# Kernel tuning notes

Measured on AMD Instinct MI355X. Metric: run time of the kernel, lower is better.

## Reference

```python
import jax, jax.numpy as jnp
import numpy as np

B, S, D = 2, 8192, 1024
H, DK, DV = 8, 64, 64
DH = 4096
SEG = 2048
NSEG = S // SEG
EPS = 1e-5


def setup_inputs() -> dict:
    key = jax.random.key(0)
    ks = jax.random.split(key, 9)
    g = lambda k, shp, sc: jax.random.normal(k, shp, jnp.float32) * sc
    return {
        "x": g(ks[0], (B, S, D), 1.0),
        "Wq": g(ks[1], (D, H * DK), 0.02),
        "Wk": g(ks[2], (D, H * DK), 0.02),
        "Wv": g(ks[3], (D, H * DV), 0.02),
        "Wo": g(ks[4], (H * DV, D), 0.02),
        "betas": g(ks[5], (1, H, 1, DV), 1.0),
        "W1": g(ks[6], (D, DH), 0.02),
        "b1": jnp.zeros((DH,), jnp.float32),
        "W2": g(ks[7], (DH, D), 0.02),
        "b2": jnp.zeros((D,), jnp.float32),
        "ln_g": jnp.ones((D,), jnp.float32),
        "ln_b": jnp.zeros((D,), jnp.float32),
    }


def _compressive_memory(x, Wq, Wk, Wv, Wo, betas):
    # project and split heads: (B, H, S, d)
    q = (x @ Wq).reshape(B, S, H, DK).transpose(0, 2, 1, 3)
    k = (x @ Wk).reshape(B, S, H, DK).transpose(0, 2, 1, 3)
    v = (x @ Wv).reshape(B, S, H, DV).transpose(0, 2, 1, 3)

    # chunk into segments: (NSEG, B, H, SEG, d)
    seg = lambda t, d: t.reshape(B, H, NSEG, SEG, d).transpose(2, 0, 1, 3, 4)
    qs, ks_, vs = seg(q, DK), seg(k, DK), seg(v, DV)

    mem0 = jnp.zeros((B, H, DK, DV), jnp.float32)
    z0 = jnp.ones((B, H, DK, 1), jnp.float32) / DK
    causal_mask = jnp.tril(jnp.ones((SEG, SEG), bool))
    scale = np.float32(1.0 / np.sqrt(DK))
    gate = jax.nn.sigmoid(betas)  # (1, H, 1, DV)

    def step(carry, inp):
        mem, z = carry
        qi, ki, vi = inp  # (B, H, SEG, d)
        sq = jax.nn.elu(qi) + 1.0
        sk = jax.nn.elu(ki) + 1.0
        # memory retrieval (uses state from previous segments)
        att_mem = (sq @ mem) / (sq @ z)  # (B, H, SEG, DV)
        # local causal SDP attention within the segment
        scores = jnp.einsum('bhqd,bhkd->bhqk', qi, ki) * scale
        scores = jnp.where(causal_mask, scores, -jnp.inf)
        att_dot = jax.nn.softmax(scores, axis=-1) @ vi
        # linear memory update
        mem = mem + jnp.einsum('bhsd,bhsv->bhdv', sk, vi)
        z = z + sk.sum(axis=-2, keepdims=True).transpose(0, 1, 3, 2)
        att = gate * att_mem + (1.0 - gate) * att_dot
        return (mem, z), att

    _, atts = jax.lax.scan(step, (mem0, z0), (qs, ks_, vs))
    # (NSEG, B, H, SEG, DV) -> (B, S, H*DV)
    att = atts.transpose(1, 0, 3, 2, 4).reshape(B, S, H * DV)
    return att @ Wo


def reference(x, Wq, Wk, Wv, Wo, betas, W1, b1, W2, b2, ln_g, ln_b):
    a = _compressive_memory(x, Wq, Wk, Wv, Wo, betas)
    h = jax.nn.gelu(a @ W1 + b1, approximate=False) @ W2 + b2
    y = h + x
    mu = y.mean(axis=-1, keepdims=True)
    var = ((y - mu) ** 2).mean(axis=-1, keepdims=True)
    return (y - mu) / jnp.sqrt(var + EPS) * ln_g + ln_b
```

## Files before the change

kernel.cpp:

```cpp
#include <hip/hip_runtime.h>
#include <hip/hip_bf16.h>
#include <math.h>

#define B_    2
#define S_    8192
#define D_    1024
#define H_N   8
#define DK_   64
#define DV_   64
#define DH_   4096
#define SEG_  2048
#define NSEG_ 4
#define EPS_  1e-5f
#define LDQKV 1536

typedef __hip_bfloat16 bf16;
typedef unsigned int u32;
typedef __attribute__((ext_vector_type(8))) short bf16x8;
typedef __attribute__((ext_vector_type(4))) float f32x4;

union bvec { bf16x8 v; bf16 e[8]; };

template <typename T> __device__ inline T from_f(float v);
template <> __device__ inline float from_f<float>(float v) { return v; }
template <> __device__ inline bf16  from_f<bf16>(float v)  { return __float2bfloat16(v); }

__device__ __forceinline__ void gld_lds16(const bf16* g, bf16* l) {
    __builtin_amdgcn_global_load_lds(
        (const __attribute__((address_space(1))) u32*)g,
        (__attribute__((address_space(3))) u32*)l, 16, 0, 0);
}

__device__ inline float elu1(float x) { return x > 0.f ? x + 1.f : __expf(x); }

#define GP(APTR, BPTR, MH, LOADB)                                              \
    {                                                                          \
        if (LOADB) {                                                           \
            _Pragma("unroll")                                                  \
            for (int n = 0; n < 4; n++)                                        \
                bg[n] = *(const bf16x8*)((BPTR) + n * 2048);                   \
        }                                                                      \
        _Pragma("unroll")                                                      \
        for (int m = 0; m < 4; m++)                                            \
            af[m] = *(const bf16x8*)((APTR) + (MH) * 8192 + m * 2048);         \
        asm volatile("s_waitcnt lgkmcnt(0)" ::: "memory");                     \
        __builtin_amdgcn_sched_barrier(0);                                     \
        __builtin_amdgcn_s_setprio(1);                                         \
        _Pragma("unroll")                                                      \
        for (int m = 0; m < 4; m++)                                            \
            _Pragma("unroll")                                                  \
            for (int n = 0; n < 4; n++)                                        \
                acc[(MH) * 4 + m][n] = __builtin_amdgcn_mfma_f32_16x16x32_bf16(\
                    af[m], bg[n], acc[(MH) * 4 + m][n], 0, 0, 0);              \
        __builtin_amdgcn_s_setprio(0);                                         \
    }

template <int EPI, typename CT>
__global__ __launch_bounds__(512, 1) void gemm256(
    const bf16* __restrict__ A, const bf16* __restrict__ BT, CT* __restrict__ C,
    const float* __restrict__ bias, const float* __restrict__ resid,
    int M, int N, int K)
{
    __shared__ bf16 L0[32768];
    __shared__ bf16 L1[32768];
    const int t    = threadIdx.x;
    const int lane = t & 63;
    const int w    = t >> 6;
    const int la   = lane & 15;
    const int g    = lane >> 4;

    const int nx  = gridDim.x;
    const int nwg = nx * gridDim.y;
    const int lin = blockIdx.y * nx + blockIdx.x;
    const int swzb = (lin & 7) * (nwg >> 3) + (lin >> 3);
    const int by  = swzb / nx, bx = swzb - by * nx;

    const int m0 = by * 256, n0 = bx * 256;
    const int wm = w >> 2, wn = w & 3;

    f32x4 acc[8][4];
    #pragma unroll
    for (int m = 0; m < 8; m++)
        #pragma unroll
        for (int n = 0; n < 4; n++) {
            f32x4 z4 = {0.f, 0.f, 0.f, 0.f};
            acc[m][n] = z4;
        }

    const int nt = K >> 6;

    const int rq = w * 8 + (lane >> 3);
    const int c8 = ((lane & 7) ^ (lane >> 3)) * 8;
    auto stageQ = [&](int kt_, int q, bf16* Lb) {
        const size_t k0 = (size_t)kt_ << 6;
        gld_lds16(A  + (size_t)(m0 + q * 64 + rq) * K + k0 + c8,
                  Lb + q * 4096 + w * 512);
        gld_lds16(BT + (size_t)(n0 + q * 64 + rq) * K + k0 + c8,
                  Lb + 16384 + q * 4096 + w * 512);
    };

    const int sw0 = (g ^ (la & 7)) << 4;
    const int sw1 = ((4 + g) ^ (la & 7)) << 4;
    const int aoff = (wm * 128 + la) * 128;
    const int boff = 32768 + (wn * 64 + la) * 128;
    const char* a0k0 = (const char*)L0 + aoff + sw0;
    const char* a0k1 = (const char*)L0 + aoff + sw1;
    const char* b0k0 = (const char*)L0 + boff + sw0;
    const char* b0k1 = (const char*)L0 + boff + sw1;
    const char* a1k0 = (const char*)L1 + aoff + sw0;
    const char* a1k1 = (const char*)L1 + aoff + sw1;
    const char* b1k0 = (const char*)L1 + boff + sw0;
    const char* b1k1 = (const char*)L1 + boff + sw1;

    stageQ(0, 0, L0); stageQ(0, 1, L0); stageQ(0, 2, L0); stageQ(0, 3, L0);

    bf16x8 af[4], bg[4];
    for (int tt = 0; tt < nt; tt += 2) {
        const bool more = (tt + 2 < nt);
        __builtin_amdgcn_s_barrier();
        stageQ(tt + 1, 0, L1);
        asm volatile("s_waitcnt vmcnt(2)" ::: "memory");
        __builtin_amdgcn_sched_barrier(0);
        __builtin_amdgcn_s_barrier();
        GP(a0k0, b0k0, 0, true);
        __builtin_amdgcn_s_barrier();
        stageQ(tt + 1, 1, L1);
        GP(a0k0, b0k0, 1, false);
        __builtin_amdgcn_s_barrier();
        stageQ(tt + 1, 2, L1);
        GP(a0k1, b0k1, 0, true);
        __builtin_amdgcn_s_barrier();
        stageQ(tt + 1, 3, L1);
        GP(a0k1, b0k1, 1, false);
        __builtin_amdgcn_s_barrier();
        if (more) {
            stageQ(tt + 2, 0, L0);
            asm volatile("s_waitcnt vmcnt(2)" ::: "memory");
        } else {
            asm volatile("s_waitcnt vmcnt(0)" ::: "memory");
        }
        __builtin_amdgcn_sched_barrier(0);
        __builtin_amdgcn_s_barrier();
        GP(a1k0, b1k0, 0, true);
        __builtin_amdgcn_s_barrier();
        if (more) stageQ(tt + 2, 1, L0);
        GP(a1k0, b1k0, 1, false);
        __builtin_amdgcn_s_barrier();
        if (more) stageQ(tt + 2, 2, L0);
        GP(a1k1, b1k1, 0, true);
        __builtin_amdgcn_s_barrier();
        if (more) stageQ(tt + 2, 3, L0);
        GP(a1k1, b1k1, 1, false);
    }

    const int row0 = m0 + wm * 128 + g * 4;
    const int col0 = n0 + wn * 64 + la;
    float bj[4];
    if (EPI >= 2) {
        #pragma unroll
        for (int n = 0; n < 4; n++) bj[n] = bias[col0 + n * 16];
    }
    #pragma unroll
    for (int m = 0; m < 8; m++) {
        #pragma unroll
        for (int r = 0; r < 4; r++) {
            const int row = row0 + m * 16 + r;
            #pragma unroll
            for (int n = 0; n < 4; n++) {
                const int col = col0 + n * 16;
                float v = acc[m][n][r];
                if (EPI >= 2) v += bj[n];
                if (EPI == 2) v = 0.5f * v * (1.0f + erff(v * 0.70710678118654752f));
                if (EPI == 3) v += resid[(size_t)row * N + col];
                C[(size_t)row * N + col] = from_f<CT>(v);
            }
        }
    }
}

__global__ __launch_bounds__(256) void castx_k(const float* __restrict__ X,
                                               bf16* __restrict__ Y)
{
    size_t i = ((size_t)blockIdx.x * 256 + threadIdx.x) * 4;
    float4 v = *(const float4*)(X + i);
    union { bf16 b[4]; unsigned long long u; } o;
    o.b[0] = __float2bfloat16(v.x);
    o.b[1] = __float2bfloat16(v.y);
    o.b[2] = __float2bfloat16(v.z);
    o.b[3] = __float2bfloat16(v.w);
    *(unsigned long long*)(Y + i) = o.u;
}

__global__ __launch_bounds__(256) void transcast_k(const float* __restrict__ W,
                                                   bf16* __restrict__ WT, int K, int N)
{
    __shared__ float tile[32][33];
    const int n0 = blockIdx.x * 32, k0 = blockIdx.y * 32;
    const int tx = threadIdx.x & 31, ty = threadIdx.x >> 5;
    #pragma unroll
    for (int i = 0; i < 32; i += 8)
        tile[ty + i][tx] = W[(size_t)(k0 + ty + i) * N + n0 + tx];
    __syncthreads();
    #pragma unroll
    for (int i = 0; i < 32; i += 8)
        WT[(size_t)(n0 + ty + i) * K + k0 + tx] = __float2bfloat16(tile[tx][ty + i]);
}

__global__ __launch_bounds__(256) void transqkv_k(
    const float* __restrict__ Wq, const float* __restrict__ Wk,
    const float* __restrict__ Wv, bf16* __restrict__ WT)
{
    __shared__ float tile[32][33];
    const float* W = (blockIdx.z == 0) ? Wq : (blockIdx.z == 1) ? Wk : Wv;
    bf16* dst = WT + (size_t)blockIdx.z * 512 * 1024;
    const int n0 = blockIdx.x * 32, k0 = blockIdx.y * 32;
    const int tx = threadIdx.x & 31, ty = threadIdx.x >> 5;
    #pragma unroll
    for (int i = 0; i < 32; i += 8)
        tile[ty + i][tx] = W[(size_t)(k0 + ty + i) * 512 + n0 + tx];
    __syncthreads();
    #pragma unroll
    for (int i = 0; i < 32; i += 8)
        dst[(size_t)(n0 + ty + i) * 1024 + k0 + tx] = __float2bfloat16(tile[tx][ty + i]);
}

__global__ __launch_bounds__(256) void vtrans_k(const bf16* __restrict__ V,
                                                bf16* __restrict__ Vt)
{
    __shared__ bf16 t_[64 * 64];
    const int t = threadIdx.x;
    const int sblk = blockIdx.x & 127;
    const int b = blockIdx.x >> 7;
    const int h = blockIdx.y;
    const bf16* src = V + ((size_t)b * S_ + sblk * 64) * LDQKV + h * 64;
    #pragma unroll
    for (int k = 0; k < 2; k++) {
        int e = t + k * 256;
        int r = e >> 3, c8 = (e & 7) * 8;
        *(bf16x8*)&t_[r * 64 + c8] = *(const bf16x8*)&src[(size_t)r * LDQKV + c8];
    }
    __syncthreads();
    const int dv = t & 63, s0 = (t >> 6) * 16;
    bf16* dst = Vt + ((size_t)(b * 8 + h) * 64 + dv) * (size_t)S_ + sblk * 64 + s0;
    bvec o0, o1;
    #pragma unroll
    for (int i = 0; i < 8; i++) {
        o0.e[i] = t_[(s0 + i) * 64 + dv];
        o1.e[i] = t_[(s0 + 8 + i) * 64 + dv];
    }
    *(bf16x8*)dst = o0.v;
    *(bf16x8*)(dst + 8) = o1.v;
}

__global__ __launch_bounds__(256) void memseg_k(
    const bf16* __restrict__ Kg, const bf16* __restrict__ Vg,
    float* __restrict__ MP, float* __restrict__ ZP)
{
    __shared__ float Ks[64][65];
    __shared__ float Vs[64][65];
    const int t = threadIdx.x, tx = t & 15, ty = t >> 4;
    const int sb = blockIdx.x;
    const int seg = sb >> 4, bh = sb & 15;
    const int b = bh >> 3, h = bh & 7;
    const int chunk = blockIdx.y;
    const size_t base = ((size_t)b * S_ + (size_t)seg * SEG_ + (size_t)chunk * 128) * LDQKV + h * 64;

    float acc[4][4] = {};
    float zacc[4]   = {};
    for (int st = 0; st < 2; st++) {
        #pragma unroll
        for (int kk = 0; kk < 2; kk++) {
            int e = t + kk * 256;
            int r = e >> 3, c8 = (e & 7) * 8;
            size_t go = base + ((size_t)st * 64 + r) * LDQKV + c8;
            bvec kv_, vv_;
            kv_.v = *(const bf16x8*)&Kg[go];
            vv_.v = *(const bf16x8*)&Vg[go];
            #pragma unroll
            for (int i = 0; i < 8; i++) {
                Ks[r][c8 + i] = elu1(__bfloat162float(kv_.e[i]));
                Vs[r][c8 + i] = __bfloat162float(vv_.e[i]);
            }
        }
        __syncthreads();
        for (int s = 0; s < 64; s++) {
            float a4[4], v4[4];
            #pragma unroll
            for (int i = 0; i < 4; i++) a4[i] = Ks[s][ty * 4 + i];
            #pragma unroll
            for (int j = 0; j < 4; j++) v4[j] = Vs[s][tx * 4 + j];
            #pragma unroll
            for (int i = 0; i < 4; i++)
                #pragma unroll
                for (int j = 0; j < 4; j++)
                    acc[i][j] += a4[i] * v4[j];
        }
        #pragma unroll
        for (int ii = 0; ii < 4; ii++) {
            int s = tx + ii * 16;
            #pragma unroll
            for (int i = 0; i < 4; i++) zacc[i] += Ks[s][ty * 4 + i];
        }
        __syncthreads();
    }
    const int slot = (seg * 16 + chunk) * 16 + bh;
    #pragma unroll
    for (int i = 0; i < 4; i++)
        #pragma unroll
        for (int j = 0; j < 4; j++)
            MP[(size_t)slot * 4096 + (ty * 4 + i) * 64 + tx * 4 + j] = acc[i][j];
    #pragma unroll
    for (int i = 0; i < 4; i++) {
        float zz = zacc[i];
        #pragma unroll
        for (int mk = 1; mk < 16; mk <<= 1) zz += __shfl_xor(zz, mk);
        if (tx == 0) ZP[slot * 64 + ty * 4 + i] = zz;
    }
}

__global__ __launch_bounds__(256) void prefix_k(
    const float* __restrict__ MP, const float* __restrict__ ZP,
    bf16* __restrict__ MST, float* __restrict__ ZS)
{
    const int bh = blockIdx.x;
    const int e  = blockIdx.y * 256 + threadIdx.x;
    const int dk = e >> 6, dv = e & 63;
    float s = 0.f;
    for (int si = 0; si < 64; si++) {
        if ((si & 15) == 0)
            MST[(size_t)((si >> 4) * 16 + bh) * 4096 + dv * 64 + dk] = __float2bfloat16(s);
        s += MP[(size_t)(si * 16 + bh) * 4096 + e];
    }
    if (blockIdx.y == 0 && threadIdx.x < 64) {
        const int dz = threadIdx.x;
        float z = 1.0f / DK_;
        for (int si = 0; si < 64; si++) {
            if ((si & 15) == 0) ZS[((si >> 4) * 16 + bh) * 64 + dz] = z;
            z += ZP[(si * 16 + bh) * 64 + dz];
        }
    }
}

template <int NG>
__device__ __forceinline__ void stageT(const bf16* gsrc, size_t stride, bf16* lds,
                                       int wave, int lane)
{
    #pragma unroll
    for (int ii = 0; ii < NG; ii++) {
        int i = wave * NG + ii;
        gld_lds16(gsrc + (size_t)(8 * i + (lane >> 3)) * stride
                        + (size_t)(((lane & 7) ^ (lane >> 3)) * 8),
                  lds + i * 512);
    }
}

__device__ __forceinline__ bf16x8 ldsw128(const bf16* base, int row, int colE)
{
    int off = row * 128 + ((colE * 2) ^ ((row & 7) << 4));
    return *(const bf16x8*)((const char*)base + off);
}

__global__ __launch_bounds__(256) void attn_k(
    const bf16* __restrict__ Qg, const bf16* __restrict__ Kg, const bf16* __restrict__ Vt,
    const bf16* __restrict__ MsT, const float* __restrict__ ZS,
    const float* __restrict__ betas, bf16* __restrict__ att)
{
    __shared__ bf16 KT[2][4096];
    __shared__ bf16 VTs[2][4096];
    __shared__ bf16 QP[8192];
    __shared__ float Zsm[64];

    const int t    = threadIdx.x;
    const int lane = t & 63;
    const int w    = t >> 6;
    const int la   = lane & 15;
    const int g    = lane >> 4;
    const int qt   = (int)gridDim.x - 1 - (int)blockIdx.x;
    const int bh   = blockIdx.y;
    const int seg  = blockIdx.z;
    const int b    = bh >> 3, h = bh & 7;

    const size_t srow = (size_t)b * S_ + (size_t)seg * SEG_;
    const bf16* qp  = Qg + (srow + (size_t)qt * 128) * LDQKV + h * 64;
    const bf16* kp  = Kg + srow * LDQKV + h * 64;
    const bf16* vtp = Vt + (size_t)bh * 64 * (size_t)S_ + (size_t)seg * SEG_;

    stageT<4>(qp, LDQKV, QP, w, lane);
    stageT<2>(kp, LDQKV, KT[0], w, lane);
    stageT<2>(vtp, S_, VTs[0], w, lane);
    if (t < 64) Zsm[t] = ZS[(seg * 16 + bh) * 64 + t];
    __syncthreads();

    bf16x8 aq[2][2];
    #pragma unroll
    for (int st = 0; st < 2; st++)
        #pragma unroll
        for (int s = 0; s < 2; s++)
            aq[st][s] = ldsw128(QP, w * 32 + st * 16 + la, s * 32 + g * 8);

    float m_[2] = {-1e30f, -1e30f};
    float l_[2] = {0.f, 0.f};
    f32x4 Oa[2][4];
    #pragma unroll
    for (int st = 0; st < 2; st++)
        #pragma unroll
        for (int j = 0; j < 4; j++) { f32x4 z4 = {0.f,0.f,0.f,0.f}; Oa[st][j] = z4; }

    const int jtmax = 2 * qt + 1;
    int cur = 0;
    for (int jt = 0; jt <= jtmax; jt++, cur ^= 1) {
        if (jt < jtmax) {
            stageT<2>(kp + (size_t)(jt + 1) * 64 * LDQKV, LDQKV, KT[cur ^ 1], w, lane);
            stageT<2>(vtp + (size_t)(jt + 1) * 64, S_, VTs[cur ^ 1], w, lane);
        }

        bf16x8 kf[2][4];
        #pragma unroll
        for (int s = 0; s < 2; s++)
            #pragma unroll
            for (int j = 0; j < 4; j++)
                kf[s][j] = ldsw128(KT[cur], j * 16 + la, s * 32 + g * 8);

        const int jtkv = jt * 64;
        #pragma unroll
        for (int st = 0; st < 2; st++) {
            f32x4 sc[4];
            #pragma unroll
            for (int j = 0; j < 4; j++) { f32x4 z4 = {0.f,0.f,0.f,0.f}; sc[j] = z4; }
            #pragma unroll
            for (int j = 0; j < 4; j++) {
                sc[j] = __builtin_amdgcn_mfma_f32_16x16x32_bf16(kf[0][j], aq[st][0], sc[j], 0, 0, 0);
                sc[j] = __builtin_amdgcn_mfma_f32_16x16x32_bf16(kf[1][j], aq[st][1], sc[j], 0, 0, 0);
            }

            const int q_abs = qt * 128 + w * 32 + st * 16 + la;
            float sv[4][4];
            float mx = -1e30f;
            #pragma unroll
            for (int j = 0; j < 4; j++)
                #pragma unroll
                for (int r = 0; r < 4; r++) {
                    float v = sc[j][r] * 0.125f;
                    int kv = jtkv + j * 16 + g * 4 + r;
                    v = (kv <= q_abs) ? v : -1e30f;
                    sv[j][r] = v;
                    mx = fmaxf(mx, v);
                }
            mx = fmaxf(mx, __shfl_xor(mx, 16));
            mx = fmaxf(mx, __shfl_xor(mx, 32));
            float mnew = fmaxf(m_[st], mx);
            float corr = __expf(m_[st] - mnew);
            float rs = 0.f;
            #pragma unroll
            for (int j = 0; j < 4; j++)
                #pragma unroll
                for (int r = 0; r < 4; r++) {
                    float p = __expf(sv[j][r] - mnew);
                    sv[j][r] = p;
                    rs += p;
                }
            rs += __shfl_xor(rs, 16);
            rs += __shfl_xor(rs, 32);
            l_[st] = l_[st] * corr + rs;
            m_[st] = mnew;

            const int R = w * 32 + st * 16 + la;
            #pragma unroll
            for (int j = 0; j < 4; j++) {
                union { bf16 e[4]; uint2 u; } pk;
                #pragma unroll
                for (int r = 0; r < 4; r++) pk.e[r] = __float2bfloat16(sv[j][r]);
                int off = R * 128 + ((j * 32 + g * 8) ^ ((la & 7) << 4));
                *(uint2*)((char*)QP + off) = pk.u;
            }

            #pragma unroll
            for (int r = 0; r < 4; r++) {
                float corr_r = __shfl(corr, (lane & 48) | (g * 4 + r));
                #pragma unroll
                for (int j = 0; j < 4; j++) Oa[st][j][r] *= corr_r;
            }
        }

        asm volatile("s_waitcnt lgkmcnt(0)" ::: "memory");
        __builtin_amdgcn_sched_barrier(0);

        bf16x8 bv[2][4];
        #pragma unroll
        for (int s = 0; s < 2; s++)
            #pragma unroll
            for (int j = 0; j < 4; j++)
                bv[s][j] = ldsw128(VTs[cur], j * 16 + la, s * 32 + g * 8);
        #pragma unroll
        for (int st = 0; st < 2; st++) {
            bf16x8 ap0 = ldsw128(QP, w * 32 + st * 16 + la, g * 8);
            bf16x8 ap1 = ldsw128(QP, w * 32 + st * 16 + la, 32 + g * 8);
            #pragma unroll
            for (int j = 0; j < 4; j++) {
                Oa[st][j] = __builtin_amdgcn_mfma_f32_16x16x32_bf16(ap0, bv[0][j], Oa[st][j], 0, 0, 0);
                Oa[st][j] = __builtin_amdgcn_mfma_f32_16x16x32_bf16(ap1, bv[1][j], Oa[st][j], 0, 0, 0);
            }
        }
        __syncthreads();
    }

    stageT<2>(MsT + (size_t)(seg * 16 + bh) * 4096, 64, KT[0], w, lane);
    __syncthreads();

    bf16x8 sq[2][2];
    float den[2] = {0.f, 0.f};
    #pragma unroll
    for (int st = 0; st < 2; st++) {
        #pragma unroll
        for (int s = 0; s < 2; s++) {
            bvec in, outv;
            in.v = aq[st][s];
            #pragma unroll
            for (int e = 0; e < 8; e++) {
                float f = elu1(__bfloat162float(in.e[e]));
                outv.e[e] = __float2bfloat16(f);
                den[st] += f * Zsm[s * 32 + 8 * g + e];
            }
            sq[st][s] = outv.v;
        }
        den[st] += __shfl_xor(den[st], 16);
        den[st] += __shfl_xor(den[st], 32);
    }

    bf16x8 bm[2][4];
    #pragma unroll
    for (int s = 0; s < 2; s++)
        #pragma unroll
        for (int j = 0; j < 4; j++)
            bm[s][j] = ldsw128(KT[0], j * 16 + la, s * 32 + g * 8);

    float gate[4];
    #pragma unroll
    for (int j = 0; j < 4; j++)
        gate[j] = 1.f / (1.f + __expf(-betas[h * 64 + j * 16 + la]));

    #pragma unroll
    for (int st = 0; st < 2; st++) {
        f32x4 num[4];
        #pragma unroll
        for (int j = 0; j < 4; j++) { f32x4 z4 = {0.f,0.f,0.f,0.f}; num[j] = z4; }
        #pragma unroll
        for (int j = 0; j < 4; j++) {
            num[j] = __builtin_amdgcn_mfma_f32_16x16x32_bf16(sq[st][0], bm[0][j], num[j], 0, 0, 0);
            num[j] = __builtin_amdgcn_mfma_f32_16x16x32_bf16(sq[st][1], bm[1][j], num[j], 0, 0, 0);
        }
        #pragma unroll
        for (int r = 0; r < 4; r++) {
            float den_r = __shfl(den[st], (lane & 48) | (g * 4 + r));
            float l_r   = __shfl(l_[st],  (lane & 48) | (g * 4 + r));
            float linv  = 1.f / l_r;
            float dinv  = 1.f / den_r;
            size_t orow = srow + (size_t)qt * 128 + w * 32 + st * 16 + g * 4 + r;
            #pragma unroll
            for (int j = 0; j < 4; j++) {
                float am = num[j][r] * dinv;
                float ad = Oa[st][j][r] * linv;
                att[orow * 512 + h * 64 + j * 16 + la] =
                    __float2bfloat16(gate[j] * am + (1.f - gate[j]) * ad);
            }
        }
    }
}

__global__ __launch_bounds__(256) void ln_k(
    const float* __restrict__ Y, const float* __restrict__ g,
    const float* __restrict__ bta, float* __restrict__ out)
{
    const int row = blockIdx.x;
    const float* yp = Y + (size_t)row * D_;
    const int t = threadIdx.x;
    float v[4];
    float s = 0.f, s2 = 0.f;
    #pragma unroll
    for (int i = 0; i < 4; i++) {
        v[i] = yp[t + i * 256];
        s += v[i]; s2 += v[i] * v[i];
    }
    #pragma unroll
    for (int mk = 1; mk < 64; mk <<= 1) {
        s  += __shfl_xor(s, mk);
        s2 += __shfl_xor(s2, mk);
    }
    __shared__ float ss[4], ss2[4];
    int w = t >> 6;
    if ((t & 63) == 0) { ss[w] = s; ss2[w] = s2; }
    __syncthreads();
    s  = ss[0] + ss[1] + ss[2] + ss[3];
    s2 = ss2[0] + ss2[1] + ss2[2] + ss2[3];
    float mu   = s / D_;
    float var  = s2 / D_ - mu * mu;
    float rstd = rsqrtf(var + EPS_);
    #pragma unroll
    for (int i = 0; i < 4; i++) {
        int c = t + i * 256;
        out[(size_t)row * D_ + c] = (v[i] - mu) * rstd * g[c] + bta[c];
    }
}

extern "C" void kernel_launch(void* const* d_in, const int* in_sizes, int n_in,
                              void* d_out, int out_size, void* d_ws, size_t ws_size,
                              hipStream_t stream)
{
    const float* x     = (const float*)d_in[0];
    const float* Wq    = (const float*)d_in[1];
    const float* Wk    = (const float*)d_in[2];
    const float* Wv    = (const float*)d_in[3];
    const float* Wo    = (const float*)d_in[4];
    const float* betas = (const float*)d_in[5];
    const float* W1    = (const float*)d_in[6];
    const float* b1    = (const float*)d_in[7];
    const float* W2    = (const float*)d_in[8];
    const float* b2    = (const float*)d_in[9];
    const float* lng   = (const float*)d_in[10];
    const float* lnb   = (const float*)d_in[11];
    float* out = (float*)d_out;

    const int M = B_ * S_;
    char* base = (char*)d_ws;
    const size_t MB = 1024 * 1024;

    bf16*  Ab    = (bf16*)(base);
    bf16*  Hb    = (bf16*)(base + 32 * MB);
    bf16*  Xbf   = (bf16*)(base + 32 * MB);
    bf16*  QKV   = (bf16*)(base + 64 * MB);
    bf16*  Vt    = (bf16*)(base + 112 * MB);
    bf16*  ATT   = (bf16*)(base + 128 * MB);
    bf16*  WqkvT = (bf16*)(base + 160 * MB);
    bf16*  WoT   = (bf16*)(base + 163 * MB);
    bf16*  W1T   = (bf16*)(base + 164 * MB);
    bf16*  W2T   = (bf16*)(base + 172 * MB);
    float* MP    = (float*)(base + 180 * MB);
    bf16*  MST   = (bf16*)(base + 196 * MB);
    float* ZP    = (float*)(base + 197 * MB);
    float* ZS    = (float*)(base + 197 * MB + 512 * 1024);

    dim3 blk(256);
    dim3 blk512(512);

    castx_k<<<dim3((M * D_) / 1024), blk, 0, stream>>>(x, Xbf);
    transqkv_k<<<dim3(16, 32, 3), blk, 0, stream>>>(Wq, Wk, Wv, WqkvT);
    transcast_k<<<dim3(1024 / 32, 512 / 32), blk, 0, stream>>>(Wo, WoT, 512, 1024);
    transcast_k<<<dim3(4096 / 32, 1024 / 32), blk, 0, stream>>>(W1, W1T, 1024, 4096);
    transcast_k<<<dim3(1024 / 32, 4096 / 32), blk, 0, stream>>>(W2, W2T, 4096, 1024);

    gemm256<0, bf16><<<dim3(1536 / 256, M / 256), blk512, 0, stream>>>(
        Xbf, WqkvT, QKV, nullptr, nullptr, M, 1536, 1024);

    vtrans_k<<<dim3(256, 8), blk, 0, stream>>>(QKV + 1024, Vt);

    memseg_k<<<dim3(NSEG_ * 16, 16), blk, 0, stream>>>(QKV + 512, QKV + 1024, MP, ZP);
    prefix_k<<<dim3(16, 16), blk, 0, stream>>>(MP, ZP, MST, ZS);

    attn_k<<<dim3(SEG_ / 128, 16, NSEG_), blk, 0, stream>>>(
        QKV, QKV + 512, Vt, MST, ZS, betas, ATT);

    gemm256<0, bf16><<<dim3(1024 / 256, M / 256), blk512, 0, stream>>>(
        ATT, WoT, Ab, nullptr, nullptr, M, 1024, 512);
    gemm256<2, bf16><<<dim3(4096 / 256, M / 256), blk512, 0, stream>>>(
        Ab, W1T, Hb, b1, nullptr, M, 4096, 1024);
    gemm256<3, float><<<dim3(1024 / 256, M / 256), blk512, 0, stream>>>(
        Hb, W2T, out, b2, x, M, 1024, 4096);

    ln_k<<<dim3(M), blk, 0, stream>>>(out, lng, lnb, out);
}
```

Baseline: 688.0 us.

## Add 128x128 GEMM for small projections and store pre-LayerNorm residual in bf16

Adds a 128x128-tile, 256-thread GEMM kernel with double-buffered LDS staging via direct global-to-LDS loads. It is used for the QKV and output projections, where the 256 tiles gave few workgroups relative to the CU count. The W2 GEMM now writes its residual sum in bf16 into a reused workspace buffer, and the LayerNorm reads bf16 with vectorized loads, cutting memory traffic. The bf16 intermediate before LayerNorm loses precision, and the workspace offsets for ZP/ZS were repacked.

```diff
diff --git a/kernel.cpp b/kernel.cpp
--- a/kernel.cpp
+++ b/kernel.cpp
@@ -32,6 +32,8 @@
 }
 
 __device__ inline float elu1(float x) { return x > 0.f ? x + 1.f : __expf(x); }
+
+#define VMC(N) asm volatile("s_waitcnt vmcnt(" #N ")" ::: "memory")
 
 #define GP(APTR, BPTR, MH, LOADB)                                              \
     {                                                                          \
@@ -178,6 +180,120 @@
     }
 }
 
+template <int EPI, typename CT>
+__global__ __launch_bounds__(256, 4) void gemm128(
+    const bf16* __restrict__ A, const bf16* __restrict__ BT, CT* __restrict__ C,
+    const float* __restrict__ bias, const float* __restrict__ resid,
+    int M, int N, int K)
+{
+    __shared__ bf16 L0[8192];
+    __shared__ bf16 L1[8192];
+    const int t    = threadIdx.x;
+    const int lane = t & 63;
+    const int w    = t >> 6;
+    const int la   = lane & 15;
+    const int g    = lane >> 4;
+
+    const int nx  = gridDim.x;
+    const int nwg = nx * gridDim.y;
+    const int lin = blockIdx.y * nx + blockIdx.x;
+    const int swzb = (lin & 7) * (nwg >> 3) + (lin >> 3);
+    const int by  = swzb / nx, bx = swzb - by * nx;
+
+    const int m0 = by * 128, n0 = bx * 128;
+    const int wm = w >> 1, wn = w & 1;
+
+    f32x4 acc[4][4];
+    #pragma unroll
+    for (int m = 0; m < 4; m++)
+        #pragma unroll
+        for (int n = 0; n < 4; n++) {
+            f32x4 z4 = {0.f, 0.f, 0.f, 0.f};
+            acc[m][n] = z4;
+        }
+
+    const int nt = K >> 5;
+
+    const int r16 = lane >> 2;
+    const int c4  = ((lane & 3) ^ ((lane >> 3) & 3)) * 8;
+    auto stage = [&](int kt_, bf16* Lb) {
+        const size_t k0 = (size_t)kt_ << 5;
+        #pragma unroll
+        for (int j = 0; j < 2; j++) {
+            const int row = (j * 4 + w) * 16 + r16;
+            gld_lds16(A  + (size_t)(m0 + row) * K + k0 + c4,
+                      Lb + (j * 4 + w) * 512);
+            gld_lds16(BT + (size_t)(n0 + row) * K + k0 + c4,
+                      Lb + 4096 + (j * 4 + w) * 512);
+        }
+    };
+
+    const int swz = ((g ^ ((la >> 1) & 3)) << 4);
+    const char* bA0 = (const char*)L0 + (wm * 64 + la) * 64 + swz;
+    const char* bB0 = (const char*)L0 + 8192 + (wn * 64 + la) * 64 + swz;
+    const char* bA1 = (const char*)L1 + (wm * 64 + la) * 64 + swz;
+    const char* bB1 = (const char*)L1 + 8192 + (wn * 64 + la) * 64 + swz;
+
+    auto comp = [&](const char* bA, const char* bB) {
+        bf16x8 af[4], bg[4];
+        #pragma unroll
+        for (int n = 0; n < 4; n++) bg[n] = *(const bf16x8*)(bB + n * 1024);
+        #pragma unroll
+        for (int m = 0; m < 4; m++) af[m] = *(const bf16x8*)(bA + m * 1024);
+        #pragma unroll
+        for (int m = 0; m < 4; m++)
+            #pragma unroll
+            for (int n = 0; n < 4; n++)
+                acc[m][n] = __builtin_amdgcn_mfma_f32_16x16x32_bf16(
+                    af[m], bg[n], acc[m][n], 0, 0, 0);
+    };
+
+    stage(0, L0);
+    VMC(0);
+    __builtin_amdgcn_sched_barrier(0);
+    __builtin_amdgcn_s_barrier();
+
+    for (int tt = 0; tt < nt; tt += 2) {
+        const bool more = (tt + 2 < nt);
+        stage(tt + 1, L1);
+        comp(bA0, bB0);
+        VMC(0);
+        __builtin_amdgcn_sched_barrier(0);
+        __builtin_amdgcn_s_barrier();
+        if (more) stage(tt + 2, L0);
+        comp(bA1, bB1);
+        if (more) {
+            VMC(0);
+            __builtin_amdgcn_sched_barrier(0);
+            __builtin_amdgcn_s_barrier();
+        }
+    }
+
+    const int row0 = m0 + wm * 64 + g * 4;
+    const int col0 = n0 + wn * 64 + la;
+    float bj[4];
+    if (EPI >= 2) {
+        #pragma unroll
+        for (int n = 0; n < 4; n++) bj[n] = bias[col0 + n * 16];
+    }
+    #pragma unroll
+    for (int m = 0; m < 4; m++) {
+        #pragma unroll
+        for (int r = 0; r < 4; r++) {
+            const int row = row0 + m * 16 + r;
+            #pragma unroll
+            for (int n = 0; n < 4; n++) {
+                const int col = col0 + n * 16;
+                float v = acc[m][n][r];
+                if (EPI >= 2) v += bj[n];
+                if (EPI == 2) v = 0.5f * v * (1.0f + erff(v * 0.70710678118654752f));
+                if (EPI == 3) v += resid[(size_t)row * N + col];
+                C[(size_t)row * N + col] = from_f<CT>(v);
+            }
+        }
+    }
+}
+
 __global__ __launch_bounds__(256) void castx_k(const float* __restrict__ X,
                                                bf16* __restrict__ Y)
 {
@@ -567,19 +683,23 @@
     }
 }
 
-__global__ __launch_bounds__(256) void ln_k(
-    const float* __restrict__ Y, const float* __restrict__ g,
+__global__ __launch_bounds__(256) void lnb_k(
+    const bf16* __restrict__ Y, const float* __restrict__ g,
     const float* __restrict__ bta, float* __restrict__ out)
 {
     const int row = blockIdx.x;
-    const float* yp = Y + (size_t)row * D_;
+    const bf16* yp = Y + (size_t)row * D_;
     const int t = threadIdx.x;
     float v[4];
     float s = 0.f, s2 = 0.f;
-    #pragma unroll
-    for (int i = 0; i < 4; i++) {
-        v[i] = yp[t + i * 256];
-        s += v[i]; s2 += v[i] * v[i];
+    {
+        union { bf16 e[4]; uint2 u; } ld;
+        ld.u = *(const uint2*)(yp + t * 4);
+        #pragma unroll
+        for (int i = 0; i < 4; i++) {
+            v[i] = __bfloat162float(ld.e[i]);
+            s += v[i]; s2 += v[i] * v[i];
+        }
     }
     #pragma unroll
     for (int mk = 1; mk < 64; mk <<= 1) {
@@ -597,7 +717,7 @@
     float rstd = rsqrtf(var + EPS_);
     #pragma unroll
     for (int i = 0; i < 4; i++) {
-        int c = t + i * 256;
+        int c = t * 4 + i;
         out[(size_t)row * D_ + c] = (v[i] - mu) * rstd * g[c] + bta[c];
     }
 }
@@ -625,6 +745,7 @@
     const size_t MB = 1024 * 1024;
 
     bf16*  Ab    = (bf16*)(base);
+    bf16*  Yb    = (bf16*)(base);
     bf16*  Hb    = (bf16*)(base + 32 * MB);
     bf16*  Xbf   = (bf16*)(base + 32 * MB);
     bf16*  QKV   = (bf16*)(base + 64 * MB);
@@ -636,8 +757,8 @@
     bf16*  W2T   = (bf16*)(base + 172 * MB);
     float* MP    = (float*)(base + 180 * MB);
     bf16*  MST   = (bf16*)(base + 196 * MB);
-    float* ZP    = (float*)(base + 197 * MB);
-    float* ZS    = (float*)(base + 197 * MB + 512 * 1024);
+    float* ZP    = (float*)(base + 196 * MB + 512 * 1024);
+    float* ZS    = (float*)(base + 196 * MB + 768 * 1024);
 
     dim3 blk(256);
     dim3 blk512(512);
@@ -648,7 +769,7 @@
     transcast_k<<<dim3(4096 / 32, 1024 / 32), blk, 0, stream>>>(W1, W1T, 1024, 4096);
     transcast_k<<<dim3(1024 / 32, 4096 / 32), blk, 0, stream>>>(W2, W2T, 4096, 1024);
 
-    gemm256<0, bf16><<<dim3(1536 / 256, M / 256), blk512, 0, stream>>>(
+    gemm128<0, bf16><<<dim3(1536 / 128, M / 128), blk, 0, stream>>>(
         Xbf, WqkvT, QKV, nullptr, nullptr, M, 1536, 1024);
 
     vtrans_k<<<dim3(256, 8), blk, 0, stream>>>(QKV + 1024, Vt);
@@ -659,12 +780,12 @@
     attn_k<<<dim3(SEG_ / 128, 16, NSEG_), blk, 0, stream>>>(
         QKV, QKV + 512, Vt, MST, ZS, betas, ATT);
 
-    gemm256<0, bf16><<<dim3(1024 / 256, M / 256), blk512, 0, stream>>>(
+    gemm128<0, bf16><<<dim3(1024 / 128, M / 128), blk, 0, stream>>>(
         ATT, WoT, Ab, nullptr, nullptr, M, 1024, 512);
     gemm256<2, bf16><<<dim3(4096 / 256, M / 256), blk512, 0, stream>>>(
         Ab, W1T, Hb, b1, nullptr, M, 4096, 1024);
-    gemm256<3, float><<<dim3(1024 / 256, M / 256), blk512, 0, stream>>>(
-        Hb, W2T, out, b2, x, M, 1024, 4096);
-
-    ln_k<<<dim3(M), blk, 0, stream>>>(out, lng, lnb, out);
-}
+    gemm256<3, bf16><<<dim3(1024 / 256, M / 256), blk512, 0, stream>>>(
+        Hb, W2T, Yb, b2, x, M, 1024, 4096);
+
+    lnb_k<<<dim3(M), blk, 0, stream>>>(Yb, lng, lnb, out);
+}
```

Measured after the change: 658.1 us (median of 2 runs). -4.3%, faster.
